# Kernel optimization log

Hardware: AMD Instinct MI355X
Metric: run time of the kernel (lower is better)

The kernel has to match this reference:

```python
import jax, jax.numpy as jnp
import numpy as np

D = 1024            # BIGNET_DIM
GS = 16             # group_size
NG = D * D // GS    # groups per layer = 65536
N_LAYERS = 18       # 6 blocks * 3 linears
LORA_LAYERS = {0: 0, 6: 1, 12: 2}  # linear index -> lora slot (first linear of blocks 0,2,4)
RANK = 32
BATCH = 16384
EPS = 1e-5


def setup_inputs() -> dict:
    key = jax.random.key(0)
    ks = jax.random.split(key, 6)
    x = jax.random.normal(ks[0], (BATCH, D), dtype=jnp.float32)
    w_q = jax.random.randint(ks[1], (N_LAYERS, NG, GS), 0, 16, dtype=jnp.int32)
    w_norm = jax.random.uniform(ks[2], (N_LAYERS, NG, 1), dtype=jnp.float32)
    bias = jax.random.normal(ks[3], (N_LAYERS, D), dtype=jnp.float32) * 0.02
    lora_a = jax.random.normal(ks[4], (3, RANK, D), dtype=jnp.float32) * (1.0 / np.sqrt(D))
    lora_b = jax.random.normal(ks[5], (3, D, RANK), dtype=jnp.float32) * 0.02
    ln_w = jnp.ones((6, D), dtype=jnp.float32)
    ln_b = jnp.zeros((6, D), dtype=jnp.float32)
    return {"x": x, "w_q": w_q, "w_norm": w_norm, "bias": bias,
            "lora_a": lora_a, "lora_b": lora_b, "ln_w": ln_w, "ln_b": ln_b}


def _dequant(q, n):
    # block_dequantize_4bit: codes in [0,15] -> [-norm, +norm] per group
    return ((q.astype(jnp.float32) / 15.0) * 2.0 - 1.0) * n  # [NG, GS]


def reference(x, w_q, w_norm, bias, lora_a, lora_b, ln_w, ln_b):
    h = x
    for blk in range(6):
        for pos in range(3):
            l = blk * 3 + pos
            W = _dequant(w_q[l], w_norm[l]).reshape(D, D)  # [out, in]
            out = h @ W.T + bias[l]
            if l in LORA_LAYERS:
                i = LORA_LAYERS[l]
                out = out + (h @ lora_a[i].T) @ lora_b[i].T
            if pos < 2:
                out = jax.nn.relu(out)
            h = out
        mu = jnp.mean(h, axis=-1, keepdims=True)
        var = jnp.mean(jnp.square(h - mu), axis=-1, keepdims=True)
        h = (h - mu) * jax.lax.rsqrt(var + EPS) * ln_w[blk] + ln_b[blk]
    return h
```

## Files before the change

kernel.cpp:

```cpp
#include <hip/hip_runtime.h>
#include <cstdint>
#include <cstddef>


typedef short  bf16x8 __attribute__((ext_vector_type(8)));
typedef float  f32x4  __attribute__((ext_vector_type(4)));

__device__ __forceinline__ unsigned short f2bf(float f) {
  unsigned int u = __builtin_bit_cast(unsigned int, f);
  u += 0x7FFFu + ((u >> 16) & 1u);
  return (unsigned short)(u >> 16);
}

__device__ __forceinline__ void async_copy16(void* lds, const void* g) {
  __builtin_amdgcn_global_load_lds(
      (const __attribute__((address_space(1))) void*)(uintptr_t)(g),
      (__attribute__((address_space(3))) void*)(unsigned int)(uintptr_t)(lds),
      16, 0, 0);
}

__global__ __launch_bounds__(256) void lora_kernel(
    const float* __restrict__ lora_a,
    const float* __restrict__ lora_b,
    float* __restrict__ LA) {
  const int slot = blockIdx.y;
  const int o0   = blockIdx.x * 4;
  const int t    = threadIdx.x;
  const float* A = lora_a + slot * 32768 + t * 4;
  const float* B = lora_b + slot * 32768 + o0 * 32;

  float acc[4][4];
#pragma unroll
  for (int k = 0; k < 4; ++k)
#pragma unroll
    for (int j = 0; j < 4; ++j) acc[k][j] = 0.f;

#pragma unroll 8
  for (int r = 0; r < 32; ++r) {
    const float4 a4 = *(const float4*)(A + r * 1024);
#pragma unroll
    for (int k = 0; k < 4; ++k) {
      const float br = B[k * 32 + r];
      acc[k][0] = fmaf(br, a4.x, acc[k][0]);
      acc[k][1] = fmaf(br, a4.y, acc[k][1]);
      acc[k][2] = fmaf(br, a4.z, acc[k][2]);
      acc[k][3] = fmaf(br, a4.w, acc[k][3]);
    }
  }
#pragma unroll
  for (int k = 0; k < 4; ++k) {
    float4 o = make_float4(acc[k][0], acc[k][1], acc[k][2], acc[k][3]);
    *(float4*)(LA + (size_t)slot * 1048576 + (size_t)(o0 + k) * 1024 + t * 4) = o;
  }
}

__global__ __launch_bounds__(256) void dequant_kernel(
    const int* __restrict__ wq, const float* __restrict__ wn,
    const float* __restrict__ LA,
    unsigned short* __restrict__ Wbf) {
  const int l   = blockIdx.y;
  const int t   = threadIdx.x;
  const int blk = blockIdx.x;
  const long base = (long)l * 1048576;
  const float s = 2.0f / 15.0f;

  const int slot = (l == 0) ? 0 : (l == 6) ? 1 : (l == 12) ? 2 : -1;

  int4  q[4];
  float nrm[4];
  float4 c4[4];
#pragma unroll
  for (int k = 0; k < 4; ++k) {
    const int i4 = blk * 1024 + k * 256 + t;
    q[k]   = *(const int4*)(wq + base + (long)i4 * 4);
    nrm[k] = wn[l * 65536 + (i4 >> 2)];
  }
  if (slot >= 0) {
    const float* LAp = LA + (size_t)slot * 1048576;
#pragma unroll
    for (int k = 0; k < 4; ++k) {
      const int i4 = blk * 1024 + k * 256 + t;
      c4[k] = *(const float4*)(LAp + (size_t)i4 * 4);
    }
  }

  float v[4][4];
#pragma unroll
  for (int k = 0; k < 4; ++k) {
    v[k][0] = ((float)q[k].x * s - 1.0f) * nrm[k];
    v[k][1] = ((float)q[k].y * s - 1.0f) * nrm[k];
    v[k][2] = ((float)q[k].z * s - 1.0f) * nrm[k];
    v[k][3] = ((float)q[k].w * s - 1.0f) * nrm[k];
  }
  if (slot >= 0) {
#pragma unroll
    for (int k = 0; k < 4; ++k) {
      v[k][0] += c4[k].x; v[k][1] += c4[k].y;
      v[k][2] += c4[k].z; v[k][3] += c4[k].w;
    }
  }

#pragma unroll
  for (int k = 0; k < 4; ++k) {
    unsigned short u[4] = {f2bf(v[k][0]), f2bf(v[k][1]),
                           f2bf(v[k][2]), f2bf(v[k][3])};
    const long e0 = base + ((long)blk * 1024 + k * 256 + t) * 4;
    *(uint2*)(Wbf + e0) = *(uint2*)u;
  }
}

__global__ __launch_bounds__(256) void cvt_bf16_kernel(
    const float* __restrict__ in, unsigned short* __restrict__ out) {
  const long b0 = (long)blockIdx.x * 4096 + threadIdx.x * 4;
  float4 v[4];
#pragma unroll
  for (int k = 0; k < 4; ++k) v[k] = *(const float4*)(in + b0 + k * 1024);
#pragma unroll
  for (int k = 0; k < 4; ++k) {
    unsigned short u[4] = {f2bf(v[k].x), f2bf(v[k].y), f2bf(v[k].z), f2bf(v[k].w)};
    *(ushort4*)(out + b0 + k * 1024) = *(ushort4*)u;
  }
}

template <int MODE>
__global__ __launch_bounds__(256, 4) void gemm_kernel(
    const unsigned short* __restrict__ H,
    const unsigned short* __restrict__ W,
    const float* __restrict__ bias,
    unsigned short* __restrict__ outb) {
  constexpr int K = 1024;
  constexpr int NN = 1024;

  __shared__ uint4 ldsq[2048];
  char* base = (char*)ldsq;

  const int tid = threadIdx.x;
  const int w   = tid >> 6;
  const int ln  = tid & 63;
  const int b   = blockIdx.x;
  const int m0  = ((b & 7) * 16 + (b >> 6)) * 128;
  const int n0  = ((b >> 3) & 7) * 128;

  const int gc = (ln & 7) ^ (ln >> 3);
  const unsigned short* gA = H + (size_t)(m0 + w * 32 + (ln >> 3)) * K + gc * 8;
  const unsigned short* gB = W + (size_t)(n0 + w * 32 + (ln >> 3)) * K + gc * 8;
  char* ldsA = base + w * 4096;
  char* ldsB = base + 16384 + w * 4096;

  const int quad = ln >> 4;
  const int lrow = ln & 15;
  const int sw   = lrow & 7;
  const int c0   = ((quad)     ^ sw) * 16;
  const int c1   = ((quad + 4) ^ sw) * 16;
  const int wm   = (w >> 1) * 64;
  const int wn   = (w & 1) * 64;
  const char* fragA = base + (wm + lrow) * 128;
  const char* fragB = base + 16384 + (wn + lrow) * 128;

  f32x4 acc[4][4];
#pragma unroll
  for (int i = 0; i < 4; ++i)
#pragma unroll
    for (int j = 0; j < 4; ++j) acc[i][j] = (f32x4){0.f, 0.f, 0.f, 0.f};

  for (int kt = 0; kt < 16; ++kt) {
    const unsigned short* pA = gA + kt * 64;
    const unsigned short* pB = gB + kt * 64;
#pragma unroll
    for (int i = 0; i < 4; ++i) {
      async_copy16(ldsA + i * 1024, pA + (size_t)i * 8 * K);
      async_copy16(ldsB + i * 1024, pB + (size_t)i * 8 * K);
    }
    __syncthreads();
#pragma unroll
    for (int kk = 0; kk < 2; ++kk) {
      const int co = kk ? c1 : c0;
      bf16x8 af[4], bg[4];
#pragma unroll
      for (int mt = 0; mt < 4; ++mt)
        af[mt] = *(const bf16x8*)(fragA + mt * 2048 + co);
#pragma unroll
      for (int nt = 0; nt < 4; ++nt)
        bg[nt] = *(const bf16x8*)(fragB + nt * 2048 + co);
#pragma unroll
      for (int mt = 0; mt < 4; ++mt)
#pragma unroll
        for (int nt = 0; nt < 4; ++nt)
          acc[mt][nt] = __builtin_amdgcn_mfma_f32_16x16x32_bf16(
              af[mt], bg[nt], acc[mt][nt], 0, 0, 0);
    }
    __syncthreads();
  }

#pragma unroll
  for (int nt = 0; nt < 4; ++nt) {
    const int n = n0 + wn + nt * 16 + lrow;
    const float bs = bias[n];
#pragma unroll
    for (int mt = 0; mt < 4; ++mt) {
      const int mb = m0 + wm + mt * 16 + quad * 4;
      f32x4 v = acc[mt][nt];
#pragma unroll
      for (int r = 0; r < 4; ++r) {
        float o = v[r] + bs;
        if (MODE == 0) o = fmaxf(o, 0.0f);
        outb[(size_t)(mb + r) * NN + n] = f2bf(o);
      }
    }
  }
}

__global__ __launch_bounds__(256) void ln_bf16_kernel(
    const unsigned short* __restrict__ in, const float* __restrict__ lnw,
    const float* __restrict__ lnb, unsigned short* __restrict__ outb,
    float* __restrict__ outf, int wbf, int wf32) {
  const int wv = threadIdx.x >> 6;
  const int ln = threadIdx.x & 63;
  const int row = blockIdx.x * 4 + wv;
  const unsigned short* p = in + (size_t)row * 1024 + ln * 16;

  const uint4 r0 = *(const uint4*)(p);
  const uint4 r1 = *(const uint4*)(p + 8);
  const unsigned ru[8] = {r0.x, r0.y, r0.z, r0.w, r1.x, r1.y, r1.z, r1.w};

  float f[16];
#pragma unroll
  for (int i = 0; i < 8; ++i) {
    f[2 * i]     = __builtin_bit_cast(float, ru[i] << 16);
    f[2 * i + 1] = __builtin_bit_cast(float, ru[i] & 0xffff0000u);
  }

  float s = 0.f, q = 0.f;
#pragma unroll
  for (int i = 0; i < 16; ++i) { s += f[i]; q += f[i] * f[i]; }
#pragma unroll
  for (int off = 32; off; off >>= 1) {
    s += __shfl_xor(s, off);
    q += __shfl_xor(q, off);
  }
  const float mu  = s * (1.0f / 1024.0f);
  const float var = q * (1.0f / 1024.0f) - mu * mu;
  const float rs  = rsqrtf(var + 1e-5f);

  const float* wp = lnw + ln * 16;
  const float* bp = lnb + ln * 16;
  float y[16];
#pragma unroll
  for (int i = 0; i < 16; ++i) y[i] = (f[i] - mu) * rs * wp[i] + bp[i];

  if (wbf) {
    unsigned o[8];
#pragma unroll
    for (int i = 0; i < 8; ++i)
      o[i] = (unsigned)f2bf(y[2 * i]) | ((unsigned)f2bf(y[2 * i + 1]) << 16);
    unsigned short* dst = outb + (size_t)row * 1024 + ln * 16;
    *(uint4*)(dst)     = make_uint4(o[0], o[1], o[2], o[3]);
    *(uint4*)(dst + 8) = make_uint4(o[4], o[5], o[6], o[7]);
  }
  if (wf32) {
    float* dst = outf + (size_t)row * 1024 + ln * 16;
#pragma unroll
    for (int c = 0; c < 4; ++c)
      *(float4*)(dst + c * 4) = make_float4(y[c * 4], y[c * 4 + 1],
                                            y[c * 4 + 2], y[c * 4 + 3]);
  }
}

extern "C" void kernel_launch(void* const* d_in, const int* in_sizes, int n_in,
                              void* d_out, int out_size, void* d_ws, size_t ws_size,
                              hipStream_t stream) {
  const float* x    = (const float*)d_in[0];
  const int*   wq   = (const int*)d_in[1];
  const float* wn   = (const float*)d_in[2];
  const float* bias = (const float*)d_in[3];
  const float* la   = (const float*)d_in[4];
  const float* lb   = (const float*)d_in[5];
  const float* lnw  = (const float*)d_in[6];
  const float* lnb  = (const float*)d_in[7];
  float* out = (float*)d_out;

  char* ws = (char*)d_ws;
  unsigned short* Wbf = (unsigned short*)ws;
  unsigned short* hA  = (unsigned short*)(ws + 37748736);
  unsigned short* hB  = (unsigned short*)(ws + 37748736 + 33554432);
  float* LA = (float*)hB;

  lora_kernel<<<dim3(256, 3), 256, 0, stream>>>(la, lb, LA);
  dequant_kernel<<<dim3(256, 18), 256, 0, stream>>>(wq, wn, LA, Wbf);
  cvt_bf16_kernel<<<4096, 256, 0, stream>>>(x, hA);

  for (int blk = 0; blk < 6; ++blk) {
    const int l = blk * 3;
    gemm_kernel<0><<<1024, 256, 0, stream>>>(
        hA, Wbf + (size_t)l * 1048576, bias + l * 1024, hB);
    gemm_kernel<0><<<1024, 256, 0, stream>>>(
        hB, Wbf + (size_t)(l + 1) * 1048576, bias + (l + 1) * 1024, hA);
    gemm_kernel<2><<<1024, 256, 0, stream>>>(
        hA, Wbf + (size_t)(l + 2) * 1048576, bias + (l + 2) * 1024, hB);
    if (blk < 5) {
      ln_bf16_kernel<<<4096, 256, 0, stream>>>(
          hB, lnw + blk * 1024, lnb + blk * 1024, hA, nullptr, 1, 0);
    } else {
      ln_bf16_kernel<<<4096, 256, 0, stream>>>(
          hB, lnw + blk * 1024, lnb + blk * 1024, nullptr, out, 0, 1);
    }
  }
}
```

Before: 944.0 us.

## Fold LayerNorm into next block's first GEMM via row stats and weight scaling

```diff
diff --git a/kernel.cpp b/kernel.cpp
--- a/kernel.cpp
+++ b/kernel.cpp
@@ -17,6 +17,11 @@
       (const __attribute__((address_space(1))) void*)(uintptr_t)(g),
       (__attribute__((address_space(3))) void*)(unsigned int)(uintptr_t)(lds),
       16, 0, 0);
+}
+
+__global__ __launch_bounds__(256) void zero_stats_kernel(float* st) {
+  const size_t i = (size_t)blockIdx.x * 256 + threadIdx.x;
+  *(float4*)(st + i * 4) = make_float4(0.f, 0.f, 0.f, 0.f);
 }
 
 __global__ __launch_bounds__(256) void lora_kernel(
@@ -57,7 +62,12 @@
 __global__ __launch_bounds__(256) void dequant_kernel(
     const int* __restrict__ wq, const float* __restrict__ wn,
     const float* __restrict__ LA,
-    unsigned short* __restrict__ Wbf) {
+    const float* __restrict__ lnw, const float* __restrict__ lnb,
+    unsigned short* __restrict__ Wbf,
+    float* __restrict__ ubuf,
+    float* __restrict__ vbuf,
+    int fold) {
+  __shared__ float red[4][4][2];
   const int l   = blockIdx.y;
   const int t   = threadIdx.x;
   const int blk = blockIdx.x;
@@ -65,6 +75,7 @@
   const float s = 2.0f / 15.0f;
 
   const int slot = (l == 0) ? 0 : (l == 6) ? 1 : (l == 12) ? 2 : -1;
+  const int fs = (fold && l > 0 && (l % 3) == 0) ? (l / 3 - 1) : -1;
 
   int4  q[4];
   float nrm[4];
@@ -100,12 +111,52 @@
     }
   }
 
+  float4 g4 = make_float4(1.f, 1.f, 1.f, 1.f);
+  float4 b4 = make_float4(0.f, 0.f, 0.f, 0.f);
+  if (fs >= 0) {
+    g4 = *(const float4*)(lnw + fs * 1024 + t * 4);
+    b4 = *(const float4*)(lnb + fs * 1024 + t * 4);
+  }
+
+  float us[4] = {0.f, 0.f, 0.f, 0.f}, vbs[4] = {0.f, 0.f, 0.f, 0.f};
 #pragma unroll
   for (int k = 0; k < 4; ++k) {
+    if (fs >= 0) {
+      vbs[k] = b4.x * v[k][0] + b4.y * v[k][1] +
+               b4.z * v[k][2] + b4.w * v[k][3];
+      v[k][0] *= g4.x; v[k][1] *= g4.y; v[k][2] *= g4.z; v[k][3] *= g4.w;
+    }
     unsigned short u[4] = {f2bf(v[k][0]), f2bf(v[k][1]),
                            f2bf(v[k][2]), f2bf(v[k][3])};
     const long e0 = base + ((long)blk * 1024 + k * 256 + t) * 4;
     *(uint2*)(Wbf + e0) = *(uint2*)u;
+    if (fs >= 0) {
+      us[k] = __builtin_bit_cast(float, (unsigned)u[0] << 16) +
+              __builtin_bit_cast(float, (unsigned)u[1] << 16) +
+              __builtin_bit_cast(float, (unsigned)u[2] << 16) +
+              __builtin_bit_cast(float, (unsigned)u[3] << 16);
+    }
+  }
+
+  if (fs >= 0) {
+    const int wv = t >> 6, lnn = t & 63;
+#pragma unroll
+    for (int k = 0; k < 4; ++k) {
+      float a = us[k], c = vbs[k];
+#pragma unroll
+      for (int off = 32; off; off >>= 1) {
+        a += __shfl_xor(a, off);
+        c += __shfl_xor(c, off);
+      }
+      if (lnn == 0) { red[wv][k][0] = a; red[wv][k][1] = c; }
+    }
+    __syncthreads();
+    if (t < 4) {
+      const float a = red[0][t][0] + red[1][t][0] + red[2][t][0] + red[3][t][0];
+      const float c = red[0][t][1] + red[1][t][1] + red[2][t][1] + red[3][t][1];
+      ubuf[fs * 1024 + blk * 4 + t] = a;
+      vbuf[fs * 1024 + blk * 4 + t] = c;
+    }
   }
 }
 
@@ -127,7 +178,10 @@
     const unsigned short* __restrict__ H,
     const unsigned short* __restrict__ W,
     const float* __restrict__ bias,
-    unsigned short* __restrict__ outb) {
+    unsigned short* __restrict__ outb,
+    float* __restrict__ st,
+    const float* __restrict__ uv,
+    const float* __restrict__ vb) {
   constexpr int K = 1024;
   constexpr int NN = 1024;
 
@@ -192,20 +246,82 @@
     __syncthreads();
   }
 
-#pragma unroll
-  for (int nt = 0; nt < 4; ++nt) {
-    const int n = n0 + wn + nt * 16 + lrow;
-    const float bs = bias[n];
+  if (MODE == 4) {
+    float mu[4][4], rs[4][4];
 #pragma unroll
     for (int mt = 0; mt < 4; ++mt) {
       const int mb = m0 + wm + mt * 16 + quad * 4;
-      f32x4 v = acc[mt][nt];
+      const float4 s01 = *(const float4*)(st + (size_t)mb * 2);
+      const float4 s23 = *(const float4*)(st + (size_t)mb * 2 + 4);
+      const float S[4] = {s01.x, s01.z, s23.x, s23.z};
+      const float Q[4] = {s01.y, s01.w, s23.y, s23.w};
 #pragma unroll
       for (int r = 0; r < 4; ++r) {
-        float o = v[r] + bs;
-        if (MODE == 0) o = fmaxf(o, 0.0f);
-        outb[(size_t)(mb + r) * NN + n] = f2bf(o);
+        const float m_ = S[r] * (1.0f / 1024.0f);
+        const float var = Q[r] * (1.0f / 1024.0f) - m_ * m_;
+        mu[mt][r] = m_;
+        rs[mt][r] = rsqrtf(var + 1e-5f);
       }
+    }
+#pragma unroll
+    for (int nt = 0; nt < 4; ++nt) {
+      const int n = n0 + wn + nt * 16 + lrow;
+      const float un = uv[n];
+      const float bs = vb[n] + bias[n];
+#pragma unroll
+      for (int mt = 0; mt < 4; ++mt) {
+        const int mb = m0 + wm + mt * 16 + quad * 4;
+        const f32x4 v = acc[mt][nt];
+#pragma unroll
+        for (int r = 0; r < 4; ++r) {
+          float o = rs[mt][r] * (v[r] - mu[mt][r] * un) + bs;
+          o = fmaxf(o, 0.0f);
+          outb[(size_t)(mb + r) * NN + n] = f2bf(o);
+        }
+      }
+    }
+  } else {
+    float ss[4][4], qq[4][4];
+    if (MODE == 3) {
+#pragma unroll
+      for (int i = 0; i < 4; ++i)
+#pragma unroll
+        for (int j = 0; j < 4; ++j) { ss[i][j] = 0.f; qq[i][j] = 0.f; }
+    }
+#pragma unroll
+    for (int nt = 0; nt < 4; ++nt) {
+      const int n = n0 + wn + nt * 16 + lrow;
+      const float bs = bias[n];
+#pragma unroll
+      for (int mt = 0; mt < 4; ++mt) {
+        const int mb = m0 + wm + mt * 16 + quad * 4;
+        const f32x4 v = acc[mt][nt];
+#pragma unroll
+        for (int r = 0; r < 4; ++r) {
+          float o = v[r] + bs;
+          if (MODE == 0) o = fmaxf(o, 0.0f);
+          outb[(size_t)(mb + r) * NN + n] = f2bf(o);
+          if (MODE == 3) { ss[mt][r] += o; qq[mt][r] += o * o; }
+        }
+      }
+    }
+    if (MODE == 3) {
+#pragma unroll
+      for (int mt = 0; mt < 4; ++mt)
+#pragma unroll
+        for (int r = 0; r < 4; ++r) {
+          float s = ss[mt][r], q = qq[mt][r];
+#pragma unroll
+          for (int off = 1; off < 16; off <<= 1) {
+            s += __shfl_xor(s, off);
+            q += __shfl_xor(q, off);
+          }
+          if (lrow == 0) {
+            const int row = m0 + wm + mt * 16 + quad * 4 + r;
+            atomicAdd(st + (size_t)row * 2,     s);
+            atomicAdd(st + (size_t)row * 2 + 1, q);
+          }
+        }
     }
   }
 }
@@ -285,24 +401,73 @@
   unsigned short* hB  = (unsigned short*)(ws + 37748736 + 33554432);
   float* LA = (float*)hB;
 
+  const size_t tail = (size_t)5 * 16384 * 2 * 4 + (size_t)2 * 5 * 1024 * 4;
+  const bool fused = ws_size >= 104857600ull + tail + 4096;
+  float* stats = nullptr; float* ubuf = nullptr; float* vbuf = nullptr;
+  if (fused) {
+    char* tp = ws + ((ws_size - tail) & ~(size_t)255);
+    stats = (float*)tp;
+    ubuf  = stats + (size_t)5 * 16384 * 2;
+    vbuf  = ubuf + 5 * 1024;
+  }
+
+  if (fused) zero_stats_kernel<<<160, 256, 0, stream>>>(stats);
   lora_kernel<<<dim3(256, 3), 256, 0, stream>>>(la, lb, LA);
-  dequant_kernel<<<dim3(256, 18), 256, 0, stream>>>(wq, wn, LA, Wbf);
+  dequant_kernel<<<dim3(256, 18), 256, 0, stream>>>(
+      wq, wn, LA, lnw, lnb, Wbf, ubuf, vbuf, fused ? 1 : 0);
   cvt_bf16_kernel<<<4096, 256, 0, stream>>>(x, hA);
 
-  for (int blk = 0; blk < 6; ++blk) {
-    const int l = blk * 3;
-    gemm_kernel<0><<<1024, 256, 0, stream>>>(
-        hA, Wbf + (size_t)l * 1048576, bias + l * 1024, hB);
-    gemm_kernel<0><<<1024, 256, 0, stream>>>(
-        hB, Wbf + (size_t)(l + 1) * 1048576, bias + (l + 1) * 1024, hA);
-    gemm_kernel<2><<<1024, 256, 0, stream>>>(
-        hA, Wbf + (size_t)(l + 2) * 1048576, bias + (l + 2) * 1024, hB);
-    if (blk < 5) {
-      ln_bf16_kernel<<<4096, 256, 0, stream>>>(
-          hB, lnw + blk * 1024, lnb + blk * 1024, hA, nullptr, 1, 0);
-    } else {
-      ln_bf16_kernel<<<4096, 256, 0, stream>>>(
-          hB, lnw + blk * 1024, lnb + blk * 1024, nullptr, out, 0, 1);
-    }
-  }
-}
+#define WL(i) (Wbf + (size_t)(i) * 1048576)
+  if (fused) {
+    gemm_kernel<0><<<1024, 256, 0, stream>>>(hA, WL(0), bias, hB,
+                                             nullptr, nullptr, nullptr);
+    gemm_kernel<0><<<1024, 256, 0, stream>>>(hB, WL(1), bias + 1024, hA,
+                                             nullptr, nullptr, nullptr);
+    gemm_kernel<3><<<1024, 256, 0, stream>>>(hA, WL(2), bias + 2048, hB,
+                                             stats, nullptr, nullptr);
+    for (int blk = 1; blk <= 4; ++blk) {
+      const int l = blk * 3;
+      unsigned short* in  = (blk & 1) ? hB : hA;
+      unsigned short* mid = (blk & 1) ? hA : hB;
+      gemm_kernel<4><<<1024, 256, 0, stream>>>(
+          in, WL(l), bias + l * 1024, mid,
+          stats + (size_t)(blk - 1) * 32768,
+          ubuf + (blk - 1) * 1024, vbuf + (blk - 1) * 1024);
+      gemm_kernel<0><<<1024, 256, 0, stream>>>(
+          mid, WL(l + 1), bias + (l + 1) * 1024, in,
+          nullptr, nullptr, nullptr);
+      gemm_kernel<3><<<1024, 256, 0, stream>>>(
+          in, WL(l + 2), bias + (l + 2) * 1024, mid,
+          stats + (size_t)blk * 32768, nullptr, nullptr);
+    }
+    gemm_kernel<4><<<1024, 256, 0, stream>>>(
+        hB, WL(15), bias + 15 * 1024, hA,
+        stats + (size_t)4 * 32768, ubuf + 4 * 1024, vbuf + 4 * 1024);
+    gemm_kernel<0><<<1024, 256, 0, stream>>>(hA, WL(16), bias + 16 * 1024, hB,
+                                             nullptr, nullptr, nullptr);
+    gemm_kernel<2><<<1024, 256, 0, stream>>>(hB, WL(17), bias + 17 * 1024, hA,
+                                             nullptr, nullptr, nullptr);
+    ln_bf16_kernel<<<4096, 256, 0, stream>>>(
+        hA, lnw + 5 * 1024, lnb + 5 * 1024, nullptr, out, 0, 1);
+  } else {
+    for (int blk = 0; blk < 6; ++blk) {
+      const int l = blk * 3;
+      gemm_kernel<0><<<1024, 256, 0, stream>>>(hA, WL(l), bias + l * 1024, hB,
+                                               nullptr, nullptr, nullptr);
+      gemm_kernel<0><<<1024, 256, 0, stream>>>(hB, WL(l + 1),
+                                               bias + (l + 1) * 1024, hA,
+                                               nullptr, nullptr, nullptr);
+      gemm_kernel<2><<<1024, 256, 0, stream>>>(hA, WL(l + 2),
+                                               bias + (l + 2) * 1024, hB,
+                                               nullptr, nullptr, nullptr);
+      if (blk < 5) {
+        ln_bf16_kernel<<<4096, 256, 0, stream>>>(
+            hB, lnw + blk * 1024, lnb + blk * 1024, hA, nullptr, 1, 0);
+      } else {
+        ln_bf16_kernel<<<4096, 256, 0, stream>>>(
+            hB, lnw + blk * 1024, lnb + blk * 1024, nullptr, out, 0, 1);
+      }
+    }
+  }
+#undef WL
+}
```

Measured after the change: 1.061 ms. 1.12x slower.
